# Optimization experiments

Measured on AMD Instinct MI355X. Metric: run time of the kernel, lower is better.

## Reference

```python
import jax, jax.numpy as jnp
import numpy as np

PATCH = 16
FEAT = 64
RADIUS = 3
EPS = 1e-06


def setup_inputs() -> dict:
    key = jax.random.key(0)
    ks = jax.random.split(key, 7)
    B, G, H, W, N = 8, 20, 512, 512, 32
    HE = jax.random.uniform(ks[0], (B, 3, H, W), jnp.float32)
    HQST = jax.random.uniform(ks[1], (B, G, H, W), jnp.float32)
    cell_mask = jax.random.randint(ks[2], (B, N, H, W), 0, 2, jnp.int32)
    w1 = jax.random.normal(ks[3], (FEAT, FEAT), jnp.float32) * 0.05
    b1 = jax.random.normal(ks[4], (FEAT,), jnp.float32) * 0.05
    w2 = jax.random.normal(ks[5], (FEAT, FEAT), jnp.float32) * 0.05
    b2 = jax.random.normal(ks[6], (FEAT,), jnp.float32) * 0.05
    return dict(HE=HE, HQST=HQST, cell_mask=cell_mask, w1=w1, b1=b1, w2=w2, b2=b2)


def _select_patch(HE):
    # vectorized per-16x16-patch Shannon entropy + argmax (replaces nested python loops)
    B, _, H, W = HE.shape
    nh, nw = H // PATCH, W // PATCH
    Np = nh * nw
    gray = 0.2989 * HE[:, 0] + 0.587 * HE[:, 1] + 0.114 * HE[:, 2]  # [B,H,W]
    pat = gray.reshape(B, nh, PATCH, nw, PATCH).transpose(0, 1, 3, 2, 4).reshape(B, Np, PATCH * PATCH)
    pat = pat - pat.min(axis=-1, keepdims=True)
    v = pat / (pat.max(axis=-1, keepdims=True) + 1e-08)
    bins = jnp.clip((v * 256.0).astype(jnp.int32), 0, 255)          # 256-bin histc over [0,1]
    flat = (jnp.arange(B * Np, dtype=jnp.int32).reshape(B, Np, 1) * 256 + bins).reshape(-1)
    counts = jnp.zeros(B * Np * 256, jnp.float32).at[flat].add(1.0).reshape(B, Np, 256)
    prob = counts / (counts.sum(axis=-1, keepdims=True) + 1e-08)
    ent = -jnp.sum(jnp.where(prob > 0, prob * jnp.log2(jnp.where(prob > 0, prob, 1.0)), 0.0), axis=-1)
    idx = jnp.argmax(ent, axis=-1)
    return idx // nw, idx % nw


def _corr(X):
    # stabilized cell-cell correlation (detached in the original -> stop_gradient)
    X = X - X.mean(axis=0, keepdims=True)
    X = X / (jnp.std(X, axis=0, keepdims=True, ddof=1) + EPS)
    corr = X @ X.T / (X.shape[1] - 1)
    return jax.lax.stop_gradient(jnp.clip(corr, -1.0, 1.0))


def _ssim(x, y, C1=0.0001, C2=0.0001):
    mu_x, mu_y = x.mean(), y.mean()
    sx, sy = jnp.var(x, ddof=1), jnp.var(y, ddof=1)
    sxy = ((x - mu_x) * (y - mu_y)).mean()
    return (2 * mu_x * mu_y + C1) * (2 * sxy + C2) / ((mu_x ** 2 + mu_y ** 2 + C1) * (sx + sy + C2))


def reference(HE, HQST, cell_mask, w1, b1, w2, b2):
    row, col = _select_patch(HE)  # [B], [B]
    ax = jnp.arange(PATCH, dtype=jnp.float32)

    def per_image(he, hq, mask, r, c):
        y0, x0 = r * PATCH, c * PATCH
        he_c = jax.lax.dynamic_slice(he, (0, y0, x0), (he.shape[0], PATCH, PATCH))
        hq_c = jax.lax.dynamic_slice(hq, (0, y0, x0), (hq.shape[0], PATCH, PATCH))
        m = jax.lax.dynamic_slice(mask, (0, y0, x0), (mask.shape[0], PATCH, PATCH)).astype(jnp.float32)
        mn = m / (m.sum(axis=(1, 2), keepdims=True) + EPS)           # [N,P,P] normalized masks
        E_HE = jnp.einsum('chw,nhw->nc', he_c, mn)                   # [N,3]
        E_HQ = jnp.einsum('ghw,nhw->ng', hq_c, mn)                   # [N,G]
        ind = (m > 0).astype(jnp.float32)
        cnt = ind.sum(axis=(1, 2))
        cx = (ind * ax[None, None, :]).sum(axis=(1, 2)) / cnt        # mean x of nonzero pixels
        cy = (ind * ax[None, :, None]).sum(axis=(1, 2)) / cnt        # mean y
        coords = jnp.stack([cx, cy], axis=1)                         # [N,2]
        d2 = jnp.sum((coords[:, None, :] - coords[None, :, :]) ** 2, axis=-1)
        dist = jnp.sqrt(jnp.maximum(d2, 0.0))
        adj = jnp.exp(-dist / (RADIUS + EPS))
        adj = adj / (adj.sum(axis=1, keepdims=True) + 1e-08)
        pad_he = jnp.pad(E_HE, ((0, 0), (0, FEAT - E_HE.shape[1])))
        pad_hq = jnp.pad(E_HQ, ((0, 0), (0, FEAT - E_HQ.shape[1])))

        def gnn(X):
            h = jax.nn.relu((adj @ X) @ w1.T + b1)
            return jax.nn.relu((adj @ h) @ w2.T + b2)

        f_he = jnp.concatenate([pad_he, gnn(pad_he)], axis=1)        # [N,2*FEAT]
        f_hq = jnp.concatenate([pad_hq, gnn(pad_hq)], axis=1)
        ssim = jnp.clip(_ssim(_corr(f_he), _corr(f_hq)), 0.0, 1.0)
        return 1.0 - ssim

    losses = jax.vmap(per_image)(HE, HQST, cell_mask, row, col)
    return losses.sum() / HE.shape[0]
```

## Files before the change

kernel.cpp:

```cpp
#include <hip/hip_runtime.h>

#define IMG_W   512
#define IMG_HW  (512*512)
#define PATCH   16
#define NPATCH  1024
#define NCELL   32
#define NG      20
#define FEAT    64
#define EPSF    1e-6f

typedef unsigned long long ull;

__device__ __forceinline__ float wave_sum(float v) {
    #pragma unroll
    for (int o = 1; o < 64; o <<= 1) v += __shfl_xor(v, o, 64);
    return v;
}

__device__ __forceinline__ float block_sum(float v, float* sP, int t) {
    #pragma unroll
    for (int o = 1; o < 64; o <<= 1) v += __shfl_xor(v, o, 64);
    __syncthreads();
    if ((t & 63) == 0) sP[t >> 6] = v;
    __syncthreads();
    return sP[0] + sP[1] + sP[2] + sP[3];
}

__global__ __launch_bounds__(256) void k_entropy(const float* __restrict__ HE,
                                                 float* __restrict__ ent) {
    __shared__ float sMn[4], sMx[4];
    __shared__ int   s_hist[256];
    __shared__ float s_red[256];
    int t   = threadIdx.x;
    int blk = blockIdx.x;
    int b   = blk >> 10;
    int p   = blk & 1023;
    int y   = (p >> 5) * PATCH + (t >> 4);
    int x   = (p & 31) * PATCH + (t & 15);
    size_t base = (size_t)b * 3 * IMG_HW + (size_t)y * IMG_W + x;
    float r  = HE[base];
    float g  = HE[base + IMG_HW];
    float bl = HE[base + 2 * IMG_HW];
    float gray = __fadd_rn(__fadd_rn(__fmul_rn(0.2989f, r), __fmul_rn(0.587f, g)),
                           __fmul_rn(0.114f, bl));
    float mn = gray, mx = gray;
    #pragma unroll
    for (int o = 1; o < 64; o <<= 1) {
        mn = fminf(mn, __shfl_xor(mn, o, 64));
        mx = fmaxf(mx, __shfl_xor(mx, o, 64));
    }
    if ((t & 63) == 0) { sMn[t >> 6] = mn; sMx[t >> 6] = mx; }
    s_hist[t] = 0;
    __syncthreads();
    mn = fminf(fminf(sMn[0], sMn[1]), fminf(sMn[2], sMn[3]));
    mx = fmaxf(fmaxf(sMx[0], sMx[1]), fmaxf(sMx[2], sMx[3]));
    float denom = __fadd_rn(__fadd_rn(mx, -mn), 1e-8f);
    float v     = __fdiv_rn(__fadd_rn(gray, -mn), denom);
    int bin = (int)__fmul_rn(v, 256.0f);
    bin = min(max(bin, 0), 255);
    atomicAdd(&s_hist[bin], 1);
    __syncthreads();
    int   c    = s_hist[t];
    float term = 0.0f;
    if (c > 0) {
        float prob = (float)c / 256.0f;
        term = prob * log2f(prob);
    }
    s_red[t] = term; __syncthreads();
    for (int s = 128; s > 0; s >>= 1) { if (t < s) s_red[t] += s_red[t+s]; __syncthreads(); }
    if (t == 0) ent[blk] = 0.0f - s_red[0];
}

__global__ __launch_bounds__(256) void k_argmax(const float* __restrict__ ent,
                                                ull* __restrict__ keys) {
    __shared__ ull sK[4];
    int t = threadIdx.x, b = blockIdx.x;
    ull best = 0ull;
    for (int i = t; i < NPATCH; i += 256) {
        float e = ent[b * NPATCH + i];
        ull k = ((ull)__float_as_uint(e) << 32)
              | (ull)(0xFFFFFFFFu - (unsigned)i);
        best = best > k ? best : k;
    }
    #pragma unroll
    for (int o = 1; o < 64; o <<= 1) {
        ull other = __shfl_xor(best, o, 64);
        best = best > other ? best : other;
    }
    if ((t & 63) == 0) sK[t >> 6] = best;
    __syncthreads();
    if (t == 0) {
        ull k = sK[0];
        for (int w = 1; w < 4; ++w) k = k > sK[w] ? k : sK[w];
        keys[b] = k;
    }
}

__global__ __launch_bounds__(256) void k_moments(
    const float* __restrict__ HE, const float* __restrict__ HQ,
    const int*   __restrict__ M,  const ull* __restrict__ keys,
    float* __restrict__ feat)
{
    __shared__ float sP[26][4];
    int t = threadIdx.x;
    int b = blockIdx.x >> 5, n = blockIdx.x & 31;
    ull key = keys[b];
    unsigned p = 0xFFFFFFFFu - (unsigned)(key & 0xFFFFFFFFull);
    int y0 = (int)(p >> 5) * PATCH;
    int x0 = (int)(p & 31) * PATCH;
    int py = t >> 4, px = t & 15;
    size_t off = (size_t)(y0 + py) * IMG_W + (x0 + px);

    float mv = (float)M[((size_t)b * NCELL + n) * IMG_HW + off];
    int w = t >> 6, lane = t & 63;
    float s0 = wave_sum(mv);
    float s1 = wave_sum(mv * (float)px);
    float s2 = wave_sum(mv * (float)py);
    if (lane == 0) { sP[0][w] = s0; sP[1][w] = s1; sP[2][w] = s2; }
    for (int c = 0; c < 23; ++c) {
        const float* cp = (c < 3) ? HE + ((size_t)b * 3 + c) * IMG_HW
                                  : HQ + ((size_t)b * NG + (c - 3)) * IMG_HW;
        float s = wave_sum(cp[off] * mv);
        if (lane == 0) sP[3 + c][w] = s;
    }
    __syncthreads();
    if (t < 25) {
        float ms = sP[0][0] + sP[0][1] + sP[0][2] + sP[0][3];
        float s;
        if (t == 0)      s = (sP[1][0]+sP[1][1]+sP[1][2]+sP[1][3]) / ms;
        else if (t == 1) s = (sP[2][0]+sP[2][1]+sP[2][2]+sP[2][3]) / ms;
        else { int q = t + 1;
               s = (sP[q][0]+sP[q][1]+sP[q][2]+sP[q][3]) / (ms + EPSF); }
        feat[((size_t)b * 25 + t) * NCELL + n] = s;
    }
}

__global__ __launch_bounds__(256) void k_gnn(
    const float* __restrict__ w1, const float* __restrict__ b1,
    const float* __restrict__ w2, const float* __restrict__ b2,
    const float* __restrict__ feat, float* __restrict__ losses)
{
    __shared__ float sF[2][NCELL * 129];
    __shared__ float sU[4160];
    __shared__ float sAdj[NCELL * 33];
    __shared__ float sCx[32], sCy[32], sRow[32];
    __shared__ float sMu[128], sSd[128];
    __shared__ float sP[4];

    int t = threadIdx.x, b = blockIdx.x;
    const float* fb = feat + (size_t)b * 25 * NCELL;

    if (t < 32) { sCx[t] = fb[t]; sCy[t] = fb[NCELL + t]; }
    for (int i = t; i < 2 * NCELL * 129; i += 256) ((float*)sF)[i] = 0.0f;
    __syncthreads();

    for (int i = t; i < 23 * NCELL; i += 256) {
        int ch = i >> 5, n = i & 31;
        float v = fb[(2 + ch) * NCELL + n];
        if (ch < 3) sF[0][n * 129 + ch]       = v;
        else        sF[1][n * 129 + (ch - 3)] = v;
    }
    for (int i = t; i < NCELL * NCELL; i += 256) {
        int ii = i >> 5, jj = i & 31;
        float dx = sCx[ii] - sCx[jj], dy = sCy[ii] - sCy[jj];
        float dist = sqrtf(fmaxf(dx * dx + dy * dy, 0.0f));
        sAdj[ii * 33 + jj] = expf(-dist / (3.0f + EPSF));
    }
    __syncthreads();
    if (t < 32) {
        float s = 0.0f;
        #pragma unroll
        for (int j = 0; j < 32; ++j) s += sAdj[t * 33 + j];
        sRow[t] = s + 1e-8f;
    }
    __syncthreads();
    for (int i = t; i < NCELL * NCELL; i += 256)
        sAdj[(i >> 5) * 33 + (i & 31)] /= sRow[i >> 5];
    __syncthreads();

    float* sT = sU;
    float* sH = sU + 2080;
    for (int m = 0; m < 2; ++m) {
        float* F = sF[m];
        for (int idx = t; idx < NCELL * FEAT; idx += 256) {
            int n = idx >> 6, f = idx & 63;
            float s = 0.0f;
            #pragma unroll
            for (int k = 0; k < 32; ++k) s += sAdj[n * 33 + k] * F[k * 129 + f];
            sT[n * 65 + f] = s;
        }
        __syncthreads();
        for (int idx = t; idx < NCELL * FEAT; idx += 256) {
            int n = idx >> 6, f = idx & 63;
            const float4* wr = (const float4*)(w1 + (size_t)f * FEAT);
            const float*  tp = &sT[n * 65];
            float s = b1[f];
            #pragma unroll
            for (int k4 = 0; k4 < 16; ++k4) {
                float4 w4 = wr[k4];
                s += tp[k4*4+0]*w4.x + tp[k4*4+1]*w4.y + tp[k4*4+2]*w4.z + tp[k4*4+3]*w4.w;
            }
            sH[n * 65 + f] = fmaxf(s, 0.0f);
        }
        __syncthreads();
        for (int idx = t; idx < NCELL * FEAT; idx += 256) {
            int n = idx >> 6, f = idx & 63;
            float s = 0.0f;
            #pragma unroll
            for (int k = 0; k < 32; ++k) s += sAdj[n * 33 + k] * sH[k * 65 + f];
            sT[n * 65 + f] = s;
        }
        __syncthreads();
        for (int idx = t; idx < NCELL * FEAT; idx += 256) {
            int n = idx >> 6, f = idx & 63;
            const float4* wr = (const float4*)(w2 + (size_t)f * FEAT);
            const float*  tp = &sT[n * 65];
            float s = b2[f];
            #pragma unroll
            for (int k4 = 0; k4 < 16; ++k4) {
                float4 w4 = wr[k4];
                s += tp[k4*4+0]*w4.x + tp[k4*4+1]*w4.y + tp[k4*4+2]*w4.z + tp[k4*4+3]*w4.w;
            }
            F[n * 129 + 64 + f] = fmaxf(s, 0.0f);
        }
        __syncthreads();
    }

    float* sC = sU;
    for (int m = 0; m < 2; ++m) {
        float* F = sF[m];
        if (t < 128) {
            float s = 0.0f;
            #pragma unroll
            for (int n2 = 0; n2 < 32; ++n2) s += F[n2 * 129 + t];
            float mu = s / 32.0f;
            float ss = 0.0f;
            #pragma unroll
            for (int n2 = 0; n2 < 32; ++n2) { float d = F[n2 * 129 + t] - mu; ss += d * d; }
            sMu[t] = mu;
            sSd[t] = sqrtf(ss / 31.0f);
        }
        __syncthreads();
        for (int i = t; i < NCELL * 128; i += 256) {
            int n2 = i >> 7, c = i & 127;
            F[n2 * 129 + c] = (F[n2 * 129 + c] - sMu[c]) / (sSd[c] + EPSF);
        }
        __syncthreads();
        for (int i = t; i < NCELL * NCELL; i += 256) {
            int ii = i >> 5, jj = i & 31;
            float s = 0.0f;
            #pragma unroll
            for (int k = 0; k < 128; ++k) s += F[ii * 129 + k] * F[jj * 129 + k];
            s /= 127.0f;
            sC[m * 1024 + i] = fminf(fmaxf(s, -1.0f), 1.0f);
        }
        __syncthreads();
    }

    float px = 0.0f, py = 0.0f;
    for (int e = t; e < 1024; e += 256) { px += sC[e]; py += sC[1024 + e]; }
    float mux = block_sum(px, sP, t) / 1024.0f;
    float muy = block_sum(py, sP, t) / 1024.0f;
    float va = 0.0f, vb = 0.0f, vc = 0.0f;
    for (int e = t; e < 1024; e += 256) {
        float dx = sC[e] - mux, dy = sC[1024 + e] - muy;
        va += dx * dx; vb += dy * dy; vc += dx * dy;
    }
    float sxv = block_sum(va, sP, t) / 1023.0f;
    float syv = block_sum(vb, sP, t) / 1023.0f;
    float sxy = block_sum(vc, sP, t) / 1024.0f;
    if (t == 0) {
        const float C1 = 1e-4f, C2 = 1e-4f;
        float ssim = (2.0f * mux * muy + C1) * (2.0f * sxy + C2)
                   / ((mux * mux + muy * muy + C1) * (sxv + syv + C2));
        ssim = fminf(fmaxf(ssim, 0.0f), 1.0f);
        losses[b] = 1.0f - ssim;
    }
}

__global__ void k_final(const float* __restrict__ losses, float* __restrict__ out, int B) {
    if (threadIdx.x == 0) {
        float s = 0.0f;
        for (int i = 0; i < B; ++i) s += losses[i];
        out[0] = s / (float)B;
    }
}

extern "C" void kernel_launch(void* const* d_in, const int* in_sizes, int n_in,
                              void* d_out, int out_size, void* d_ws, size_t ws_size,
                              hipStream_t stream) {
    const float* HE = (const float*)d_in[0];
    const float* HQ = (const float*)d_in[1];
    const int*   M  = (const int*)d_in[2];
    const float* w1 = (const float*)d_in[3];
    const float* b1 = (const float*)d_in[4];
    const float* w2 = (const float*)d_in[5];
    const float* b2 = (const float*)d_in[6];
    float* out = (float*)d_out;

    int B = in_sizes[0] / (3 * IMG_HW);

    float* ent    = (float*)d_ws;
    ull*   keys   = (ull*)((char*)d_ws + (size_t)B * NPATCH * 4);
    float* losses = (float*)((char*)keys + (size_t)B * 8);
    float* feat   = (float*)((char*)losses + (size_t)B * 4);

    hipLaunchKernelGGL(k_entropy, dim3(B * NPATCH), dim3(256), 0, stream, HE, ent);
    hipLaunchKernelGGL(k_argmax,  dim3(B),          dim3(256), 0, stream, ent, keys);
    hipLaunchKernelGGL(k_moments, dim3(B * NCELL),  dim3(256), 0, stream, HE, HQ, M, keys, feat);
    hipLaunchKernelGGL(k_gnn,     dim3(B),          dim3(256), 0, stream, w1, b1, w2, b2, feat, losses);
    hipLaunchKernelGGL(k_final,   dim3(1),          dim3(1),   0, stream, losses, out, B);
}
```

Before: 451.2 us.

## Process one patch per wavefront in entropy and fuse argmax into moments

After: 448.3 us. About the same (-0.6%).

```diff
diff --git a/kernel.cpp b/kernel.cpp
--- a/kernel.cpp
+++ b/kernel.cpp
@@ -28,53 +28,72 @@
 
 __global__ __launch_bounds__(256) void k_entropy(const float* __restrict__ HE,
                                                  float* __restrict__ ent) {
-    __shared__ float sMn[4], sMx[4];
-    __shared__ int   s_hist[256];
-    __shared__ float s_red[256];
-    int t   = threadIdx.x;
-    int blk = blockIdx.x;
-    int b   = blk >> 10;
-    int p   = blk & 1023;
-    int y   = (p >> 5) * PATCH + (t >> 4);
-    int x   = (p & 31) * PATCH + (t & 15);
-    size_t base = (size_t)b * 3 * IMG_HW + (size_t)y * IMG_W + x;
-    float r  = HE[base];
-    float g  = HE[base + IMG_HW];
-    float bl = HE[base + 2 * IMG_HW];
-    float gray = __fadd_rn(__fadd_rn(__fmul_rn(0.2989f, r), __fmul_rn(0.587f, g)),
-                           __fmul_rn(0.114f, bl));
-    float mn = gray, mx = gray;
+    __shared__ int hist[4][256];
+    int t = threadIdx.x;
+    int w = t >> 6, l = t & 63;
+    int pid = blockIdx.x * 4 + w;
+    int b  = pid >> 10;
+    int p  = pid & 1023;
+    int pr = p >> 5, pc = p & 31;
+    int r  = l >> 2, q = l & 3;
+    size_t base = (size_t)b * 3 * IMG_HW
+                + (size_t)(pr * PATCH + r) * IMG_W + pc * PATCH + q * 4;
+    float4 cr = *(const float4*)(HE + base);
+    float4 cg = *(const float4*)(HE + base + IMG_HW);
+    float4 cb = *(const float4*)(HE + base + 2 * IMG_HW);
+    float gray[4];
+    gray[0] = __fadd_rn(__fadd_rn(__fmul_rn(0.2989f, cr.x), __fmul_rn(0.587f, cg.x)),
+                        __fmul_rn(0.114f, cb.x));
+    gray[1] = __fadd_rn(__fadd_rn(__fmul_rn(0.2989f, cr.y), __fmul_rn(0.587f, cg.y)),
+                        __fmul_rn(0.114f, cb.y));
+    gray[2] = __fadd_rn(__fadd_rn(__fmul_rn(0.2989f, cr.z), __fmul_rn(0.587f, cg.z)),
+                        __fmul_rn(0.114f, cb.z));
+    gray[3] = __fadd_rn(__fadd_rn(__fmul_rn(0.2989f, cr.w), __fmul_rn(0.587f, cg.w)),
+                        __fmul_rn(0.114f, cb.w));
+    float mn = fminf(fminf(gray[0], gray[1]), fminf(gray[2], gray[3]));
+    float mx = fmaxf(fmaxf(gray[0], gray[1]), fmaxf(gray[2], gray[3]));
     #pragma unroll
     for (int o = 1; o < 64; o <<= 1) {
         mn = fminf(mn, __shfl_xor(mn, o, 64));
         mx = fmaxf(mx, __shfl_xor(mx, o, 64));
     }
-    if ((t & 63) == 0) { sMn[t >> 6] = mn; sMx[t >> 6] = mx; }
-    s_hist[t] = 0;
-    __syncthreads();
-    mn = fminf(fminf(sMn[0], sMn[1]), fminf(sMn[2], sMn[3]));
-    mx = fmaxf(fmaxf(sMx[0], sMx[1]), fmaxf(sMx[2], sMx[3]));
     float denom = __fadd_rn(__fadd_rn(mx, -mn), 1e-8f);
-    float v     = __fdiv_rn(__fadd_rn(gray, -mn), denom);
-    int bin = (int)__fmul_rn(v, 256.0f);
-    bin = min(max(bin, 0), 255);
-    atomicAdd(&s_hist[bin], 1);
-    __syncthreads();
-    int   c    = s_hist[t];
-    float term = 0.0f;
-    if (c > 0) {
-        float prob = (float)c / 256.0f;
-        term = prob * log2f(prob);
-    }
-    s_red[t] = term; __syncthreads();
-    for (int s = 128; s > 0; s >>= 1) { if (t < s) s_red[t] += s_red[t+s]; __syncthreads(); }
-    if (t == 0) ent[blk] = 0.0f - s_red[0];
-}
-
-__global__ __launch_bounds__(256) void k_argmax(const float* __restrict__ ent,
-                                                ull* __restrict__ keys) {
+    int* h = hist[w];
+    h[l] = 0; h[l + 64] = 0; h[l + 128] = 0; h[l + 192] = 0;
+    #pragma unroll
+    for (int j = 0; j < 4; ++j) {
+        float v = __fdiv_rn(__fadd_rn(gray[j], -mn), denom);
+        int bin = (int)__fmul_rn(v, 256.0f);
+        bin = min(max(bin, 0), 255);
+        atomicAdd(&h[bin], 1);
+    }
+    float f[4];
+    #pragma unroll
+    for (int j = 0; j < 4; ++j) {
+        int c = h[l + j * 64];
+        float term = 0.0f;
+        if (c > 0) {
+            float prob = (float)c / 256.0f;
+            term = prob * log2f(prob);
+        }
+        f[j] = term;
+    }
+    float s = __fadd_rn(__fadd_rn(f[0], f[2]), __fadd_rn(f[1], f[3]));
+    #pragma unroll
+    for (int o = 32; o >= 1; o >>= 1) s = __fadd_rn(s, __shfl_xor(s, o, 64));
+    if (l == 0) ent[pid] = 0.0f - s;
+}
+
+__global__ __launch_bounds__(256) void k_moments(
+    const float* __restrict__ HE, const float* __restrict__ HQ,
+    const int*   __restrict__ M,  const float* __restrict__ ent,
+    float* __restrict__ feat)
+{
+    __shared__ float sP[26][4];
     __shared__ ull sK[4];
-    int t = threadIdx.x, b = blockIdx.x;
+    int t = threadIdx.x;
+    int b = blockIdx.x >> 5, n = blockIdx.x & 31;
+
     ull best = 0ull;
     for (int i = t; i < NPATCH; i += 256) {
         float e = ent[b * NPATCH + i];
@@ -89,22 +108,10 @@
     }
     if ((t & 63) == 0) sK[t >> 6] = best;
     __syncthreads();
-    if (t == 0) {
-        ull k = sK[0];
-        for (int w = 1; w < 4; ++w) k = k > sK[w] ? k : sK[w];
-        keys[b] = k;
-    }
-}
-
-__global__ __launch_bounds__(256) void k_moments(
-    const float* __restrict__ HE, const float* __restrict__ HQ,
-    const int*   __restrict__ M,  const ull* __restrict__ keys,
-    float* __restrict__ feat)
-{
-    __shared__ float sP[26][4];
-    int t = threadIdx.x;
-    int b = blockIdx.x >> 5, n = blockIdx.x & 31;
-    ull key = keys[b];
+    ull key = sK[0];
+    #pragma unroll
+    for (int wv = 1; wv < 4; ++wv) key = key > sK[wv] ? key : sK[wv];
+
     unsigned p = 0xFFFFFFFFu - (unsigned)(key & 0xFFFFFFFFull);
     int y0 = (int)(p >> 5) * PATCH;
     int x0 = (int)(p & 31) * PATCH;
@@ -129,8 +136,8 @@
         float s;
         if (t == 0)      s = (sP[1][0]+sP[1][1]+sP[1][2]+sP[1][3]) / ms;
         else if (t == 1) s = (sP[2][0]+sP[2][1]+sP[2][2]+sP[2][3]) / ms;
-        else { int q = t + 1;
-               s = (sP[q][0]+sP[q][1]+sP[q][2]+sP[q][3]) / (ms + EPSF); }
+        else { int q2 = t + 1;
+               s = (sP[q2][0]+sP[q2][1]+sP[q2][2]+sP[q2][3]) / (ms + EPSF); }
         feat[((size_t)b * 25 + t) * NCELL + n] = s;
     }
 }
@@ -301,13 +308,11 @@
     int B = in_sizes[0] / (3 * IMG_HW);
 
     float* ent    = (float*)d_ws;
-    ull*   keys   = (ull*)((char*)d_ws + (size_t)B * NPATCH * 4);
-    float* losses = (float*)((char*)keys + (size_t)B * 8);
+    float* losses = (float*)((char*)d_ws + (size_t)B * NPATCH * 4);
     float* feat   = (float*)((char*)losses + (size_t)B * 4);
 
-    hipLaunchKernelGGL(k_entropy, dim3(B * NPATCH), dim3(256), 0, stream, HE, ent);
-    hipLaunchKernelGGL(k_argmax,  dim3(B),          dim3(256), 0, stream, ent, keys);
-    hipLaunchKernelGGL(k_moments, dim3(B * NCELL),  dim3(256), 0, stream, HE, HQ, M, keys, feat);
-    hipLaunchKernelGGL(k_gnn,     dim3(B),          dim3(256), 0, stream, w1, b1, w2, b2, feat, losses);
-    hipLaunchKernelGGL(k_final,   dim3(1),          dim3(1),   0, stream, losses, out, B);
-}
+    hipLaunchKernelGGL(k_entropy, dim3(B * NPATCH / 4), dim3(256), 0, stream, HE, ent);
+    hipLaunchKernelGGL(k_moments, dim3(B * NCELL),      dim3(256), 0, stream, HE, HQ, M, ent, feat);
+    hipLaunchKernelGGL(k_gnn,     dim3(B),              dim3(256), 0, stream, w1, b1, w2, b2, feat, losses);
+    hipLaunchKernelGGL(k_final,   dim3(1),              dim3(1),   0, stream, losses, out, B);
+}
```
